# Kernel tuning notes

Measured on AMD Instinct MI355X. Metric: run time of the kernel, lower is better.

Reference implementation:

```python
import jax, jax.numpy as jnp
import numpy as np

N_NODES = 100000
N_EDGES = 1600000
IN_DIM = 128
HID = 64
OUT_DIM = 1


def setup_inputs() -> dict:
    key = jax.random.key(0)
    ks = jax.random.split(key, 8)
    x = jax.random.normal(ks[0], (N_NODES, IN_DIM), dtype=jnp.float32)
    edge_index = jax.random.randint(ks[1], (2, N_EDGES), 0, N_NODES, dtype=jnp.int64)
    s_in = 1.0 / np.sqrt(IN_DIM)
    s_h = 1.0 / np.sqrt(HID)
    W_in = jax.random.uniform(ks[2], (IN_DIM, HID), jnp.float32, -s_in, s_in)
    b_in = jax.random.uniform(ks[3], (HID,), jnp.float32, -s_in, s_in)
    W_g = jax.random.uniform(ks[4], (HID, HID), jnp.float32, -s_h, s_h)
    b_g = jnp.zeros((HID,), jnp.float32)
    W_out = jax.random.uniform(ks[5], (HID, OUT_DIM), jnp.float32, -s_h, s_h)
    b_out = jax.random.uniform(ks[6], (OUT_DIM,), jnp.float32, -s_h, s_h)
    return {"x": x, "edge_index": edge_index, "W_in": W_in, "b_in": b_in,
            "W_g": W_g, "b_g": b_g, "W_out": W_out, "b_out": b_out}


def _gcn_conv(h, src, dst, W, b, n_nodes):
    # GCNConv: add self-loops, symmetric normalization, sum aggregation
    loops = jnp.arange(n_nodes, dtype=src.dtype)
    src = jnp.concatenate([src, loops])
    dst = jnp.concatenate([dst, loops])
    hw = h @ W  # [N, out]
    deg = jax.ops.segment_sum(jnp.ones_like(dst, dtype=hw.dtype), dst,
                              num_segments=n_nodes)  # >=1 due to self-loops
    dinv = jax.lax.rsqrt(deg)
    norm = dinv[src] * dinv[dst]  # [E+N]
    msg = hw[src] * norm[:, None]  # gather (memory-bound)
    out = jax.ops.segment_sum(msg, dst, num_segments=n_nodes)  # scatter-add
    return out + b


def reference(x, edge_index, W_in, b_in, W_g, b_g, W_out, b_out):
    n_nodes = x.shape[0]
    h = jax.nn.relu(x @ W_in + b_in)  # input_proj + ReLU (dropout = id in eval)
    # single GCN layer (last layer -> no ReLU/dropout after)
    h = _gcn_conv(h, edge_index[0], edge_index[1], W_g, b_g, n_nodes)
    return h @ W_out + b_out  # [N, 1]
```

## Files before the change

kernel.cpp:

```cpp
#include <hip/hip_runtime.h>

#define HID 64
#define IN_DIM 128
#define RANGE_BITS 14
#define RANGE (1 << RANGE_BITS)
#define NB 7
#define MCH 36
#define SCAN_TPB 512
#define RB2 15
#define RANGE2 (1 << RB2)
#define NB2 4
#define MCH2 64
#define DNODES 64
#define SK 32
#define NCH (IN_DIM / SK)
#define LDSP (DNODES + 1)

__global__ __launch_bounds__(256) void k_dense(const float* __restrict__ x,
                                               const float* __restrict__ W_in,
                                               const float* __restrict__ b_in,
                                               const float* __restrict__ W_g,
                                               const float* __restrict__ W_out,
                                               const unsigned* __restrict__ partA,
                                               float* __restrict__ dinv,
                                               float* __restrict__ zs,
                                               int N) {
    __shared__ float weff_l[HID];
    __shared__ float ldsT[SK][LDSP];
    __shared__ float zp[4][DNODES];

    const int t = threadIdx.x;

    {
        const float* wg = W_g + (t >> 2) * HID + (t & 3) * 16;
        const float* wo = W_out + (t & 3) * 16;
        float s = 0.0f;
#pragma unroll
        for (int p = 0; p < 16; ++p) s = fmaf(wg[p], wo[p], s);
        s += __shfl_xor(s, 1, 64);
        s += __shfl_xor(s, 2, 64);
        if ((t & 3) == 0) weff_l[t >> 2] = s;
    }

    const int q = __builtin_amdgcn_readfirstlane(t >> 6);
    const int nidx = t & 63;
    const int row0 = blockIdx.x * DNODES;
    int node = row0 + nidx;
    if (node >= N) node = N - 1;

    float acc[16];
#pragma unroll
    for (int jj = 0; jj < 16; ++jj)
        acc[jj] = b_in[q * 16 + jj];

    float4 rg[2];
    const int lrow = t >> 3;
    const int lcol = (t & 7) * 4;

#define LOADC(c)                                                                 \
    {                                                                            \
        _Pragma("unroll")                                                        \
        for (int s = 0; s < 2; ++s) {                                            \
            int grow = row0 + s * 32 + lrow;                                     \
            if (grow >= N) grow = N - 1;                                         \
            rg[s] = *(const float4*)(x + (size_t)grow * IN_DIM + (c) * SK + lcol); \
        }                                                                        \
    }
#define WRITEC()                                                                 \
    {                                                                            \
        _Pragma("unroll")                                                        \
        for (int s = 0; s < 2; ++s) {                                            \
            ldsT[lcol + 0][s * 32 + lrow] = rg[s].x;                             \
            ldsT[lcol + 1][s * 32 + lrow] = rg[s].y;                             \
            ldsT[lcol + 2][s * 32 + lrow] = rg[s].z;                             \
            ldsT[lcol + 3][s * 32 + lrow] = rg[s].w;                             \
        }                                                                        \
    }

    LOADC(0);
    for (int c = 0; c < NCH; ++c) {
        WRITEC();
        __syncthreads();
        if (c + 1 < NCH) LOADC(c + 1);
#pragma unroll 8
        for (int kk = 0; kk < SK; ++kk) {
            float xv = ldsT[kk][nidx];
            const float* wr = W_in + (c * SK + kk) * HID + q * 16;
#pragma unroll
            for (int jj = 0; jj < 16; ++jj)
                acc[jj] = fmaf(xv, wr[jj], acc[jj]);
        }
        __syncthreads();
    }
#undef LOADC
#undef WRITEC

    float zv = 0.0f;
#pragma unroll
    for (int jj = 0; jj < 16; ++jj)
        zv = fmaf(fmaxf(acc[jj], 0.0f), weff_l[q * 16 + jj], zv);
    zp[q][nidx] = zv;
    __syncthreads();

    if (t < 64) {
        float z = zp[0][t] + zp[1][t] + zp[2][t] + zp[3][t];
        const int n = node;
        const int r = n >> RB2, idx = n & (RANGE2 - 1);
        const int sh = (idx & 1) << 4;
        const unsigned* base = partA + (size_t)r * (RANGE2 / 2) + (idx >> 1);
        const size_t stride = (size_t)NB2 * (RANGE2 / 2);
        int d = 0;
#pragma unroll 8
        for (int m = 0; m < MCH2; ++m)
            d += (int)((base[m * stride] >> sh) & 0xFFFFu);
        float di = rsqrtf((float)d + 1.0f);
        dinv[n] = di;
        zs[n]   = z * di;
    }
}

__global__ __launch_bounds__(SCAN_TPB) void k_binA(const int* __restrict__ dst,
                                                   unsigned* __restrict__ partA,
                                                   int E, int chunkA) {
    __shared__ unsigned cnt[RANGE2 / 2];
    for (int i = threadIdx.x; i < RANGE2 / 2; i += SCAN_TPB) cnt[i] = 0;
    __syncthreads();

    const int r = blockIdx.x % NB2;
    const int lo = r << RB2;
    const int e0 = (blockIdx.x / NB2) * chunkA;
    const int e1 = min(E, e0 + chunkA);
    for (int e = e0 + (int)threadIdx.x * 4; e + 3 < e1; e += SCAN_TPB * 4) {
        int4 d4 = *(const int4*)(dst + e);
        unsigned v;
        v = (unsigned)(d4.x - lo); if (v < RANGE2) atomicAdd(&cnt[v >> 1], 1u << ((v & 1) << 4));
        v = (unsigned)(d4.y - lo); if (v < RANGE2) atomicAdd(&cnt[v >> 1], 1u << ((v & 1) << 4));
        v = (unsigned)(d4.z - lo); if (v < RANGE2) atomicAdd(&cnt[v >> 1], 1u << ((v & 1) << 4));
        v = (unsigned)(d4.w - lo); if (v < RANGE2) atomicAdd(&cnt[v >> 1], 1u << ((v & 1) << 4));
    }
    __syncthreads();

    unsigned* outp = partA + (size_t)blockIdx.x * (RANGE2 / 2);
    for (int i = threadIdx.x; i < RANGE2 / 2; i += SCAN_TPB) outp[i] = cnt[i];
}

__global__ __launch_bounds__(SCAN_TPB) void k_binC(const int* __restrict__ eidx,
                                                   const float* __restrict__ zs,
                                                   float* __restrict__ partf,
                                                   int E, int chunk) {
    __shared__ float acc[RANGE];
    for (int i = threadIdx.x; i < RANGE; i += SCAN_TPB) acc[i] = 0.0f;
    __syncthreads();

    const int r = blockIdx.x % NB;
    const int lo = r << RANGE_BITS;
    const int e0 = (blockIdx.x / NB) * chunk;
    const int e1 = min(E, e0 + chunk);
    for (int e = e0 + (int)threadIdx.x * 4; e + 3 < e1; e += SCAN_TPB * 4) {
        int4 s4 = *(const int4*)(eidx + e);
        int4 d4 = *(const int4*)(eidx + E + e);
        unsigned v;
        v = (unsigned)(d4.x - lo); if (v < RANGE) atomicAdd(&acc[v], zs[s4.x]);
        v = (unsigned)(d4.y - lo); if (v < RANGE) atomicAdd(&acc[v], zs[s4.y]);
        v = (unsigned)(d4.z - lo); if (v < RANGE) atomicAdd(&acc[v], zs[s4.z]);
        v = (unsigned)(d4.w - lo); if (v < RANGE) atomicAdd(&acc[v], zs[s4.w]);
    }
    __syncthreads();

    float* outp = partf + (size_t)blockIdx.x * RANGE;
    for (int i = threadIdx.x; i < RANGE; i += SCAN_TPB) outp[i] = acc[i];
}

__global__ __launch_bounds__(256) void k_redFinal(const float* __restrict__ partf,
                                                  const float* __restrict__ dinv,
                                                  const float* __restrict__ zs,
                                                  const float* __restrict__ b_g,
                                                  const float* __restrict__ W_out,
                                                  const float* __restrict__ b_out,
                                                  float* __restrict__ out, int N) {
    const int lane = threadIdx.x & 63;
    float c = b_g[lane] * W_out[lane];
#pragma unroll
    for (int off = 32; off > 0; off >>= 1)
        c += __shfl_xor(c, off, 64);
    c += b_out[0];

    int i = blockIdx.x * blockDim.x + threadIdx.x;
    if (i >= N) return;
    const int r = i >> RANGE_BITS, idx = i & (RANGE - 1);
    float a = zs[i];
#pragma unroll 4
    for (int m = 0; m < MCH; ++m)
        a += partf[((size_t)m * NB + r) * RANGE + idx];
    out[i] = fmaf(dinv[i], a, c);
}


extern "C" void kernel_launch(void* const* d_in, const int* in_sizes, int n_in,
                              void* d_out, int out_size, void* d_ws, size_t ws_size,
                              hipStream_t stream) {
    const float* x     = (const float*)d_in[0];
    const int*   eidx  = (const int*)d_in[1];
    const float* W_in  = (const float*)d_in[2];
    const float* b_in  = (const float*)d_in[3];
    const float* W_g   = (const float*)d_in[4];
    const float* b_g   = (const float*)d_in[5];
    const float* W_out = (const float*)d_in[6];
    const float* b_out = (const float*)d_in[7];
    float* out = (float*)d_out;

    const int N = in_sizes[0] / IN_DIM;
    const int E = in_sizes[1] / 2;

    const int chunk  = (((E + MCH  - 1) / MCH ) + 3) & ~3;
    const int chunkA = (((E + MCH2 - 1) / MCH2) + 3) & ~3;

    const size_t partElems0 = (size_t)NB * MCH * RANGE;
    const size_t partElemsA = (size_t)NB2 * MCH2 * (RANGE2 / 2);
    const size_t partElems = partElems0 > partElemsA ? partElems0 : partElemsA;
    unsigned* partA = (unsigned*)d_ws;
    float*    partf = (float*)d_ws;
    float*    dinv  = (float*)d_ws + partElems;
    float*    zs    = dinv + N;

    const int nG = (N + DNODES - 1) / DNODES;
    k_binA<<<NB2 * MCH2, SCAN_TPB, 0, stream>>>(eidx + E, partA, E, chunkA);
    k_dense<<<nG, 256, 0, stream>>>(x, W_in, b_in, W_g, W_out, partA, dinv, zs, N);
    k_binC<<<NB * MCH, SCAN_TPB, 0, stream>>>(eidx, zs, partf, E, chunk);
    k_redFinal<<<(N + 255) / 256, 256, 0, stream>>>(partf, dinv, zs, b_g, W_out, b_out, out, N);
}
```

Baseline: 80.38 us.

## Compute input projection with bf16 MFMA instead of scalar FP32 FMAs

Replaces the scalar FP32 x@W_in loop in the dense kernel with bf16 MFMA 16x16x32 instructions. A new prep kernel transposes W_in and converts it to bf16, and each block loads its whole 64x128 x tile up front, converts it to bf16 into LDS, and reduces the ReLU·weff dot via shuffles. This removes the multi-chunk LDS transpose loop and most of the FMA work. It adds a small extra launch and lowers precision to bf16 on the inputs.

```diff
diff --git a/kernel.cpp b/kernel.cpp
--- a/kernel.cpp
+++ b/kernel.cpp
@@ -1,4 +1,7 @@
 #include <hip/hip_runtime.h>
+
+typedef __attribute__((ext_vector_type(8))) short bf16x8;
+typedef __attribute__((ext_vector_type(4))) float f32x4;
 
 #define HID 64
 #define IN_DIM 128
@@ -12,12 +15,24 @@
 #define NB2 4
 #define MCH2 64
 #define DNODES 64
-#define SK 32
-#define NCH (IN_DIM / SK)
-#define LDSP (DNODES + 1)
+#define LDSXP 136
+
+__device__ __forceinline__ unsigned short f2bf(float f) {
+    unsigned u = __builtin_bit_cast(unsigned, f);
+    return (unsigned short)((u + 0x7FFFu + ((u >> 16) & 1u)) >> 16);
+}
+
+__global__ __launch_bounds__(256) void k_prep(const float* __restrict__ W_in,
+                                              unsigned short* __restrict__ Wt) {
+    int i = blockIdx.x * 256 + threadIdx.x;
+    if (i < IN_DIM * HID) {
+        int j = i >> 7, k = i & 127;
+        Wt[i] = f2bf(W_in[k * HID + j]);
+    }
+}
 
 __global__ __launch_bounds__(256) void k_dense(const float* __restrict__ x,
-                                               const float* __restrict__ W_in,
+                                               const unsigned short* __restrict__ Wt,
                                                const float* __restrict__ b_in,
                                                const float* __restrict__ W_g,
                                                const float* __restrict__ W_out,
@@ -26,10 +41,27 @@
                                                float* __restrict__ zs,
                                                int N) {
     __shared__ float weff_l[HID];
-    __shared__ float ldsT[SK][LDSP];
-    __shared__ float zp[4][DNODES];
+    __shared__ float bl[HID];
+    __shared__ unsigned short ldsX[DNODES * LDSXP];
+    __shared__ float zp[DNODES];
 
     const int t = threadIdx.x;
+    const int row0 = blockIdx.x * DNODES;
+
+    float4 rg[8];
+    const int lrow = t >> 3;
+    const int lcol = (t & 7) * 4;
+    {
+        int gr0 = row0 + lrow;        if (gr0 >= N) gr0 = N - 1;
+        int gr1 = row0 + 32 + lrow;   if (gr1 >= N) gr1 = N - 1;
+        const float* p0 = x + (size_t)gr0 * IN_DIM + lcol;
+        const float* p1 = x + (size_t)gr1 * IN_DIM + lcol;
+#pragma unroll
+        for (int c = 0; c < 4; ++c) {
+            rg[c * 2 + 0] = *(const float4*)(p0 + c * 32);
+            rg[c * 2 + 1] = *(const float4*)(p1 + c * 32);
+        }
+    }
 
     {
         const float* wg = W_g + (t >> 2) * HID + (t & 3) * 16;
@@ -40,71 +72,74 @@
         s += __shfl_xor(s, 1, 64);
         s += __shfl_xor(s, 2, 64);
         if ((t & 3) == 0) weff_l[t >> 2] = s;
-    }
-
-    const int q = __builtin_amdgcn_readfirstlane(t >> 6);
-    const int nidx = t & 63;
-    const int row0 = blockIdx.x * DNODES;
-    int node = row0 + nidx;
-    if (node >= N) node = N - 1;
-
-    float acc[16];
-#pragma unroll
-    for (int jj = 0; jj < 16; ++jj)
-        acc[jj] = b_in[q * 16 + jj];
-
-    float4 rg[2];
-    const int lrow = t >> 3;
-    const int lcol = (t & 7) * 4;
-
-#define LOADC(c)                                                                 \
-    {                                                                            \
-        _Pragma("unroll")                                                        \
-        for (int s = 0; s < 2; ++s) {                                            \
-            int grow = row0 + s * 32 + lrow;                                     \
-            if (grow >= N) grow = N - 1;                                         \
-            rg[s] = *(const float4*)(x + (size_t)grow * IN_DIM + (c) * SK + lcol); \
-        }                                                                        \
-    }
-#define WRITEC()                                                                 \
-    {                                                                            \
-        _Pragma("unroll")                                                        \
-        for (int s = 0; s < 2; ++s) {                                            \
-            ldsT[lcol + 0][s * 32 + lrow] = rg[s].x;                             \
-            ldsT[lcol + 1][s * 32 + lrow] = rg[s].y;                             \
-            ldsT[lcol + 2][s * 32 + lrow] = rg[s].z;                             \
-            ldsT[lcol + 3][s * 32 + lrow] = rg[s].w;                             \
-        }                                                                        \
-    }
-
-    LOADC(0);
-    for (int c = 0; c < NCH; ++c) {
-        WRITEC();
-        __syncthreads();
-        if (c + 1 < NCH) LOADC(c + 1);
-#pragma unroll 8
-        for (int kk = 0; kk < SK; ++kk) {
-            float xv = ldsT[kk][nidx];
-            const float* wr = W_in + (c * SK + kk) * HID + q * 16;
-#pragma unroll
-            for (int jj = 0; jj < 16; ++jj)
-                acc[jj] = fmaf(xv, wr[jj], acc[jj]);
-        }
-        __syncthreads();
-    }
-#undef LOADC
-#undef WRITEC
-
-    float zv = 0.0f;
-#pragma unroll
-    for (int jj = 0; jj < 16; ++jj)
-        zv = fmaf(fmaxf(acc[jj], 0.0f), weff_l[q * 16 + jj], zv);
-    zp[q][nidx] = zv;
+        if (t < HID) bl[t] = b_in[t];
+    }
+
+    const int w    = __builtin_amdgcn_readfirstlane(t >> 6);
+    const int lane = t & 63;
+
+    bf16x8 bfr[4][4];
+    {
+        const int col = lane & 15;
+        const int ko  = (lane >> 4) * 8;
+#pragma unroll
+        for (int nf = 0; nf < 4; ++nf)
+#pragma unroll
+            for (int kk = 0; kk < 4; ++kk)
+                bfr[nf][kk] = *(const bf16x8*)(Wt + (size_t)(nf * 16 + col) * IN_DIM + kk * 32 + ko);
+    }
+
+#pragma unroll
+    for (int c = 0; c < 4; ++c) {
+        float4 v0 = rg[c * 2 + 0], v1 = rg[c * 2 + 1];
+        ushort4 h0 = { f2bf(v0.x), f2bf(v0.y), f2bf(v0.z), f2bf(v0.w) };
+        ushort4 h1 = { f2bf(v1.x), f2bf(v1.y), f2bf(v1.z), f2bf(v1.w) };
+        *(ushort4*)&ldsX[lrow * LDSXP + c * 32 + lcol]        = h0;
+        *(ushort4*)&ldsX[(32 + lrow) * LDSXP + c * 32 + lcol] = h1;
+    }
+    __syncthreads();
+
+    f32x4 acc[4] = {{0,0,0,0},{0,0,0,0},{0,0,0,0},{0,0,0,0}};
+    {
+        const int arow = w * 16 + (lane & 15);
+        const int ko   = (lane >> 4) * 8;
+#pragma unroll
+        for (int kk = 0; kk < 4; ++kk) {
+            bf16x8 af = *(const bf16x8*)&ldsX[arow * LDSXP + kk * 32 + ko];
+#pragma unroll
+            for (int nf = 0; nf < 4; ++nf)
+                acc[nf] = __builtin_amdgcn_mfma_f32_16x16x32_bf16(af, bfr[nf][kk], acc[nf], 0, 0, 0);
+        }
+    }
+
+    {
+        float p[4] = {0.f, 0.f, 0.f, 0.f};
+#pragma unroll
+        for (int nf = 0; nf < 4; ++nf) {
+            const int col = nf * 16 + (lane & 15);
+            const float bc = bl[col], wc = weff_l[col];
+#pragma unroll
+            for (int r = 0; r < 4; ++r)
+                p[r] = fmaf(fmaxf(acc[nf][r] + bc, 0.0f), wc, p[r]);
+        }
+#pragma unroll
+        for (int r = 0; r < 4; ++r) {
+            p[r] += __shfl_xor(p[r], 1, 64);
+            p[r] += __shfl_xor(p[r], 2, 64);
+            p[r] += __shfl_xor(p[r], 4, 64);
+            p[r] += __shfl_xor(p[r], 8, 64);
+        }
+        if ((lane & 15) == 0) {
+#pragma unroll
+            for (int r = 0; r < 4; ++r)
+                zp[w * 16 + (lane >> 4) * 4 + r] = p[r];
+        }
+    }
     __syncthreads();
 
     if (t < 64) {
-        float z = zp[0][t] + zp[1][t] + zp[2][t] + zp[3][t];
-        const int n = node;
+        int n = row0 + t; if (n >= N) n = N - 1;
+        float z = zp[t];
         const int r = n >> RB2, idx = n & (RANGE2 - 1);
         const int sh = (idx & 1) << 4;
         const unsigned* base = partA + (size_t)r * (RANGE2 / 2) + (idx >> 1);
@@ -222,10 +257,12 @@
     float*    partf = (float*)d_ws;
     float*    dinv  = (float*)d_ws + partElems;
     float*    zs    = dinv + N;
+    unsigned short* Wt = (unsigned short*)(zs + N);
 
     const int nG = (N + DNODES - 1) / DNODES;
+    k_prep<<<(IN_DIM * HID + 255) / 256, 256, 0, stream>>>(W_in, Wt);
     k_binA<<<NB2 * MCH2, SCAN_TPB, 0, stream>>>(eidx + E, partA, E, chunkA);
-    k_dense<<<nG, 256, 0, stream>>>(x, W_in, b_in, W_g, W_out, partA, dinv, zs, N);
+    k_dense<<<nG, 256, 0, stream>>>(x, Wt, b_in, W_g, W_out, partA, dinv, zs, N);
     k_binC<<<NB * MCH, SCAN_TPB, 0, stream>>>(eidx, zs, partf, E, chunk);
     k_redFinal<<<(N + 255) / 256, 256, 0, stream>>>(partf, dinv, zs, b_g, W_out, b_out, out, N);
 }
```

Result: no change. 81.80 us (+1.8%).
